# Performance work log

Hardware: AMD Instinct MI355X
Metric: run time of the kernel (lower is better)

The kernel has to match this reference:

```python
import jax, jax.numpy as jnp
import numpy as np

B, S, D, H = 8, 128, 256, 8
T = S + 1
HD = D // H  # head_dim = 32
GAMMA = 1.0
NEG_INF = -1e9
LN_EPS = 1e-5


def setup_inputs() -> dict:
    key = jax.random.key(0)
    ks = jax.random.split(key, 16)
    sc = 0.05
    return {
        "desc_embeddings": jax.random.normal(ks[0], (B, S, D), jnp.float32),
        "name_value_embeddings": jax.random.normal(ks[1], (B, T, D), jnp.float32),
        "prior_Q": jax.random.uniform(ks[2], (B, H, S, S), jnp.float32),
        "Wq": jax.random.normal(ks[3], (D, D), jnp.float32) * sc,
        "bq": jnp.zeros((D,), jnp.float32),
        "Wk": jax.random.normal(ks[4], (D, D), jnp.float32) * sc,
        "bk": jnp.zeros((D,), jnp.float32),
        "Wv": jax.random.normal(ks[5], (D, D), jnp.float32) * sc,
        "bv": jnp.zeros((D,), jnp.float32),
        "wa": jax.random.normal(ks[6], (3 * HD,), jnp.float32) * sc,  # attn_proj weight (out=1)
        "ba": jnp.zeros((), jnp.float32),
        "We1": jax.random.normal(ks[7], (2 * D, D), jnp.float32) * sc,
        "be1": jnp.zeros((D,), jnp.float32),
        "ln_g": jnp.ones((D,), jnp.float32),
        "ln_b": jnp.zeros((D,), jnp.float32),
        "We2": jax.random.normal(ks[8], (D, D), jnp.float32) * sc,
        "be2": jnp.zeros((D,), jnp.float32),
    }


def _layer_norm(x, g, b):
    mu = jnp.mean(x, axis=-1, keepdims=True)
    var = jnp.mean(jnp.square(x - mu), axis=-1, keepdims=True)
    return (x - mu) * jax.lax.rsqrt(var + LN_EPS) * g + b


def _heads(x, W, b):  # [B,T,D] -> [B,H,T,HD]
    return (x @ W + b).reshape(B, T, H, HD).transpose(0, 2, 1, 3)


def reference(desc_embeddings, name_value_embeddings, prior_Q,
              Wq, bq, Wk, bk, Wv, bv, wa, ba,
              We1, be1, ln_g, ln_b, We2, be2):
    # structural adjacency (same for every batch element): CLS->Var on, Var->CLS off,
    # Var-Var fully connected without self-loops
    adj = jnp.zeros((T, T), jnp.float32)
    adj = adj.at[1:, 1:].set(1.0 - jnp.eye(S, dtype=jnp.float32))
    adj = adj.at[0, 1:].set(1.0)

    q = _heads(name_value_embeddings, Wq, bq)  # [B,H,T,HD]
    k = _heads(name_value_embeddings, Wk, bk)
    v = _heads(name_value_embeddings, Wv, bv)

    # edge attributes: pairwise concat of desc embeddings, CLS rows/cols use [desc,desc]
    desc = desc_embeddings
    var_edge = jnp.concatenate([
        jnp.broadcast_to(desc[:, :, None, :], (B, S, S, D)),
        jnp.broadcast_to(desc[:, None, :, :], (B, S, S, D)),
    ], axis=-1)  # [B,S,S,2D]
    cls_edge = jnp.concatenate([desc, desc], axis=-1)  # [B,S,2D]
    edge = jnp.zeros((B, T, T, 2 * D), jnp.float32)
    edge = edge.at[:, 1:, 1:].set(var_edge)
    edge = edge.at[:, 0, 1:].set(cls_edge)
    edge = edge.at[:, 1:, 0].set(cls_edge)

    # edge_update MLP: Linear(2D->D) -> LayerNorm -> ReLU -> Linear(D->D)
    h = jax.nn.relu(_layer_norm(edge @ We1 + be1, ln_g, ln_b)) @ We2 + be2  # [B,T,T,D]
    # split into heads, mask by adjacency: [B,H,T,T,HD]
    edge_h = h.reshape(B, T, T, H, HD).transpose(0, 3, 1, 2, 4)
    edge_h = edge_h * adj[None, None, :, :, None]

    # gat_v1 + attn_proj(cat[q_i, k_j, e_ij]) is linear -> decompose to avoid
    # materializing the [B,H,T,T,3*HD] concat
    wa_q, wa_k, wa_e = wa[:HD], wa[HD:2 * HD], wa[2 * HD:]
    logits = (jnp.einsum('bhid,d->bhi', q, wa_q)[:, :, :, None]
              + jnp.einsum('bhjd,d->bhj', k, wa_k)[:, :, None, :]
              + jnp.einsum('bhijd,d->bhij', edge_h, wa_e)
              + ba)  # [B,H,T,T]

    # prior_Q logit-bias injection on Var-Var block
    eps = 1e-6
    p = jnp.clip(prior_Q, eps, 1.0 - eps)
    bias = (jnp.log(p) - jnp.log(1.0 - p)) * GAMMA  # [B,H,S,S]
    logits = logits.at[:, :, 1:, 1:].add(bias)

    # structural mask as pre-softmax -inf
    logits = logits + (adj == 0).astype(logits.dtype)[None, None] * NEG_INF

    attn = jax.nn.softmax(logits, axis=-1)  # [B,H,T,T]
    ctx = jnp.einsum('bhij,bhjd->bhid', attn, v)  # [B,H,T,HD]
    basis_outputs = ctx.transpose(0, 2, 1, 3)  # [B,T,H,HD]
    return basis_outputs, attn
```

## Files before the change

### kernel.cpp

```cpp
#include <hip/hip_runtime.h>
#include <math.h>

#define B 8
#define S 128
#define D 256
#define H 8
#define T 129
#define HD 32
#define NEG_INF -1000000000.0f
#define LN_EPS 1e-5f

__global__ __launch_bounds__(256) void gemm_all(
    const float* __restrict__ nv, const float* __restrict__ desc,
    const float* __restrict__ Wq, const float* __restrict__ bq,
    const float* __restrict__ Wk, const float* __restrict__ bk,
    const float* __restrict__ Wv, const float* __restrict__ bv,
    const float* __restrict__ We1, const float* __restrict__ be1,
    const float* __restrict__ We2, const float* __restrict__ be2,
    const float* __restrict__ wa,
    float* __restrict__ v, float* __restrict__ U, float* __restrict__ V,
    float* __restrict__ Vt, float* __restrict__ qdkd,
    float* __restrict__ W2aT, float* __restrict__ econst,
    float* __restrict__ sU, float* __restrict__ sU2,
    float* __restrict__ sV, float* __restrict__ sV2)
{
    const int blk = blockIdx.x;
    const int tid = threadIdx.x;

    __shared__ float xs16[16 * 260];
    __shared__ float wq_s[4096];
    __shared__ float bq_s[16];
    __shared__ float red[4][8];

    if (blk < 770) {
        const float* X; const float* W; const float* bias; int r0; int mode;
        if (blk < 258)      { X = nv;   W = Wv;        bias = bv;      r0 = blk * 4;         mode = 0; }
        else if (blk < 514) { X = desc; W = We1;       bias = be1;     r0 = (blk - 258) * 4; mode = 1; }
        else                { X = desc; W = We1 + D*D; bias = nullptr; r0 = (blk - 514) * 4; mode = 2; }
        const int c = tid;

        const float* x0 = X + (r0 + 0) * D;
        const float* x1 = X + (r0 + 1) * D;
        const float* x2 = X + (r0 + 2) * D;
        const float* x3 = X + (r0 + 3) * D;

        float acc0 = 0.f, acc1 = 0.f, acc2 = 0.f, acc3 = 0.f;
        float w[8], nw[8];
        #pragma unroll
        for (int q = 0; q < 8; ++q) w[q] = W[q * D + c];

        for (int kk = 0; kk < 256; kk += 8) {
            const int kn = kk + 8;
            if (kn < 256) {
                #pragma unroll
                for (int q = 0; q < 8; ++q) nw[q] = W[(kn + q) * D + c];
            }
            float xv0[8], xv1[8], xv2[8], xv3[8];
            *(float4*)&xv0[0] = *(const float4*)(x0 + kk);
            *(float4*)&xv0[4] = *(const float4*)(x0 + kk + 4);
            *(float4*)&xv1[0] = *(const float4*)(x1 + kk);
            *(float4*)&xv1[4] = *(const float4*)(x1 + kk + 4);
            *(float4*)&xv2[0] = *(const float4*)(x2 + kk);
            *(float4*)&xv2[4] = *(const float4*)(x2 + kk + 4);
            *(float4*)&xv3[0] = *(const float4*)(x3 + kk);
            *(float4*)&xv3[4] = *(const float4*)(x3 + kk + 4);
            #pragma unroll
            for (int q = 0; q < 8; ++q) {
                acc0 = fmaf(xv0[q], w[q], acc0);
                acc1 = fmaf(xv1[q], w[q], acc1);
                acc2 = fmaf(xv2[q], w[q], acc2);
                acc3 = fmaf(xv3[q], w[q], acc3);
            }
            if (kn < 256) {
                #pragma unroll
                for (int q = 0; q < 8; ++q) w[q] = nw[q];
            }
        }

        const float bb = bias ? bias[c] : 0.f;
        const float o0 = acc0 + bb, o1 = acc1 + bb, o2 = acc2 + bb, o3 = acc3 + bb;

        if (mode == 0) {
            if (r0 + 0 < B*T) v[(r0 + 0) * D + c] = o0;
            if (r0 + 1 < B*T) v[(r0 + 1) * D + c] = o1;
            if (r0 + 2 < B*T) v[(r0 + 2) * D + c] = o2;
            if (r0 + 3 < B*T) v[(r0 + 3) * D + c] = o3;
        } else {
            if (mode == 1) {
                U[(r0 + 0) * D + c] = o0;
                U[(r0 + 1) * D + c] = o1;
                U[(r0 + 2) * D + c] = o2;
                U[(r0 + 3) * D + c] = o3;
            } else {
                V[(r0 + 0) * D + c] = o0;
                V[(r0 + 1) * D + c] = o1;
                V[(r0 + 2) * D + c] = o2;
                V[(r0 + 3) * D + c] = o3;
                const int b_ = r0 >> 7, rl = r0 & 127;
                float4 tv; tv.x = o0; tv.y = o1; tv.z = o2; tv.w = o3;
                *(float4*)&Vt[((size_t)b_ * D + c) * S + rl] = tv;
            }
            float s0 = o0, s1 = o1, s2 = o2, s3 = o3;
            float q0 = o0*o0, q1 = o1*o1, q2 = o2*o2, q3 = o3*o3;
            #pragma unroll
            for (int m = 32; m >= 1; m >>= 1) {
                s0 += __shfl_xor(s0, m); q0 += __shfl_xor(q0, m);
                s1 += __shfl_xor(s1, m); q1 += __shfl_xor(q1, m);
                s2 += __shfl_xor(s2, m); q2 += __shfl_xor(q2, m);
                s3 += __shfl_xor(s3, m); q3 += __shfl_xor(q3, m);
            }
            const int wv = tid >> 6;
            if ((tid & 63) == 0) {
                red[wv][0] = s0; red[wv][1] = s1; red[wv][2] = s2; red[wv][3] = s3;
                red[wv][4] = q0; red[wv][5] = q1; red[wv][6] = q2; red[wv][7] = q3;
            }
            __syncthreads();
            if (tid < 4) {
                const float ss = red[0][tid] + red[1][tid] + red[2][tid] + red[3][tid];
                const float qq = red[0][4+tid] + red[1][4+tid] + red[2][4+tid] + red[3][4+tid];
                const int row = r0 + tid;
                if (mode == 1) { sU[row] = ss; sU2[row] = qq; }
                else           { sV[row] = ss; sV2[row] = qq; }
            }
        }
    } else if (blk < 835) {
        const int r0 = (blk - 770) * 16;
        for (int t = tid; t < 4096; t += 256) {
            const int k = t >> 4, cc = t & 15;
            const float* Wsrc = (cc < 8) ? Wq : Wk;
            const float* wap  = (cc < 8) ? wa : wa + HD;
            const int h = cc & 7;
            float s = 0.f;
            #pragma unroll
            for (int d = 0; d < HD; ++d) s = fmaf(Wsrc[k*D + h*HD + d], wap[d], s);
            wq_s[t] = s;
        }
        if (tid < 16) {
            const float* bsrc = (tid < 8) ? bq : bk;
            const float* wap  = (tid < 8) ? wa : wa + HD;
            const int h = tid & 7;
            float s = 0.f;
            #pragma unroll
            for (int d = 0; d < HD; ++d) s = fmaf(bsrc[h*HD + d], wap[d], s);
            bq_s[tid] = s;
        }
        for (int t = tid; t < 16 * 256; t += 256) {
            const int r = t >> 8, cch = t & 255, rr = r0 + r;
            xs16[r * 260 + cch] = (rr < B*T) ? nv[rr * D + cch] : 0.f;
        }
        __syncthreads();

        const int r = tid >> 4, cc = tid & 15;
        float acc = 0.f;
        for (int kk = 0; kk < 256; kk += 4) {
            const float4 x = *(const float4*)&xs16[r * 260 + kk];
            acc = fmaf(x.x, wq_s[(kk+0)*16 + cc], acc);
            acc = fmaf(x.y, wq_s[(kk+1)*16 + cc], acc);
            acc = fmaf(x.z, wq_s[(kk+2)*16 + cc], acc);
            acc = fmaf(x.w, wq_s[(kk+3)*16 + cc], acc);
        }
        const int rr = r0 + r;
        if (rr < B*T) qdkd[rr * 16 + cc] = acc + bq_s[cc];
    } else {
        for (int t = tid; t < 2048; t += 256) {
            const int h = t >> 8, cch = t & 255;
            float s = 0.f;
            #pragma unroll
            for (int d = 0; d < HD; ++d) s = fmaf(We2[cch*D + h*HD + d], wa[2*HD + d], s);
            W2aT[h*D + cch] = s;
        }
        if (tid < 8) {
            float s = 0.f;
            #pragma unroll
            for (int d = 0; d < HD; ++d) s = fmaf(be2[tid*HD + d], wa[2*HD + d], s);
            econst[tid] = s;
        }
    }
}

__global__ __launch_bounds__(256) void uv_gemm(
    const float* __restrict__ U, const float* __restrict__ Vt,
    float* __restrict__ UV)
{
    const int br = blockIdx.x;
    const int b  = br >> 7;
    const int j  = threadIdx.x & 127, kh = threadIdx.x >> 7;
    const float* urow = U + (size_t)br * D + kh * 128;
    const float* vt   = Vt + (size_t)b * D * S + (size_t)kh * 128 * S;

    float acc = 0.f;
    #pragma unroll 8
    for (int c = 0; c < 128; c += 4) {
        const float4 u4 = *(const float4*)(urow + c);
        acc = fmaf(u4.x, vt[(c+0)*S + j], acc);
        acc = fmaf(u4.y, vt[(c+1)*S + j], acc);
        acc = fmaf(u4.z, vt[(c+2)*S + j], acc);
        acc = fmaf(u4.w, vt[(c+3)*S + j], acc);
    }
    __shared__ float part[2][128];
    part[kh][j] = acc;
    __syncthreads();
    if (kh == 0) UV[(size_t)br * S + j] = part[0][j] + part[1][j];
}

__global__ __launch_bounds__(512) void edge_attn(
    const float* __restrict__ U, const float* __restrict__ V,
    const float* __restrict__ W2aT, const float* __restrict__ econst,
    const float* __restrict__ ln_g, const float* __restrict__ ln_b,
    const float* __restrict__ qdkd, const float* __restrict__ prior,
    const float* __restrict__ v, const float* __restrict__ ba,
    const float* __restrict__ sU, const float* __restrict__ sU2,
    const float* __restrict__ sV, const float* __restrict__ sV2,
    const float* __restrict__ UV,
    float* __restrict__ out_basis, float* __restrict__ out_attn)
{
    const int bid = blockIdx.x;
    const int b = bid / T, i = bid % T;
    const int tid = threadIdx.x, lane = tid & 63, wid = tid >> 6;
    const int c0 = lane * 4;

    __shared__ float escl[H][132];
    __shared__ float pat[H][132];

    const float4 g4 = *(const float4*)(ln_g + c0);
    const float4 b4 = *(const float4*)(ln_b + c0);
    float4 w[H];
    #pragma unroll
    for (int h = 0; h < H; ++h) w[h] = *(const float4*)(W2aT + h*D + c0);
    float4 u4i = make_float4(0.f, 0.f, 0.f, 0.f);
    float su_i = 0.f, su2_i = 0.f;
    const float* UVrow = UV;
    if (i >= 1) {
        u4i   = *(const float4*)(U + (size_t)(b*S + (i-1))*D + c0);
        su_i  = sU [b*S + i-1];
        su2_i = sU2[b*S + i-1];
        UVrow = UV + (size_t)(b*S + (i-1))*S;
    }

    const int hmap = 4*(lane&1) + 2*((lane>>1)&1) + ((lane>>2)&1);
    const float ecl = (lane < 8) ? econst[hmap] : 0.f;

    const int j0 = 1 + wid * 16;
    for (int jj = 0; jj < 16; ++jj) {
        const int j = j0 + jj;
        if (i >= 1 && j == i) continue;

        const float svj  = sV [b*S + j-1];
        const float sv2j = sV2[b*S + j-1];
        float suv, su2v, cross;
        if (i >= 1) {
            suv = su_i; su2v = su2_i;
            cross = UVrow[j-1];
        } else {
            suv   = sU [b*S + j-1];
            su2v  = sU2[b*S + j-1];
            cross = UV[(size_t)(b*S + j-1)*S + (j-1)];
        }
        const float mu  = (suv + svj) * (1.f / D);
        const float ey2 = fmaf(2.f, cross, su2v + sv2j) * (1.f / D);
        const float rs  = rsqrtf(ey2 - mu*mu + LN_EPS);

        const float4 v4 = *(const float4*)(V + (size_t)(b*S + (j-1))*D + c0);
        float4 u4;
        if (i == 0) u4 = *(const float4*)(U + (size_t)(b*S + (j-1))*D + c0);
        else        u4 = u4i;

        const float y0 = u4.x + v4.x, y1 = u4.y + v4.y;
        const float y2 = u4.z + v4.z, y3 = u4.w + v4.w;

        const float t0 = fmaxf((y0 - mu) * rs * g4.x + b4.x, 0.f);
        const float t1 = fmaxf((y1 - mu) * rs * g4.y + b4.y, 0.f);
        const float t2 = fmaxf((y2 - mu) * rs * g4.z + b4.z, 0.f);
        const float t3 = fmaxf((y3 - mu) * rs * g4.w + b4.w, 0.f);

        float ph[H];
        #pragma unroll
        for (int h = 0; h < H; ++h)
            ph[h] = fmaf(t0, w[h].x, fmaf(t1, w[h].y, fmaf(t2, w[h].z, t3 * w[h].w)));

        {
            const bool hi = (lane & 1);
            float k0 = hi ? ph[4] : ph[0], d0 = hi ? ph[0] : ph[4];
            float k1 = hi ? ph[5] : ph[1], d1 = hi ? ph[1] : ph[5];
            float k2 = hi ? ph[6] : ph[2], d2 = hi ? ph[2] : ph[6];
            float k3 = hi ? ph[7] : ph[3], d3 = hi ? ph[3] : ph[7];
            ph[0] = k0 + __shfl_xor(d0, 1);
            ph[1] = k1 + __shfl_xor(d1, 1);
            ph[2] = k2 + __shfl_xor(d2, 1);
            ph[3] = k3 + __shfl_xor(d3, 1);
        }
        {
            const bool hi = (lane & 2);
            float k0 = hi ? ph[2] : ph[0], d0 = hi ? ph[0] : ph[2];
            float k1 = hi ? ph[3] : ph[1], d1 = hi ? ph[1] : ph[3];
            ph[0] = k0 + __shfl_xor(d0, 2);
            ph[1] = k1 + __shfl_xor(d1, 2);
        }
        {
            const bool hi = (lane & 4);
            float k0 = hi ? ph[1] : ph[0], d0 = hi ? ph[0] : ph[1];
            ph[0] = k0 + __shfl_xor(d0, 4);
        }
        ph[0] += __shfl_xor(ph[0], 8);
        ph[0] += __shfl_xor(ph[0], 16);
        ph[0] += __shfl_xor(ph[0], 32);

        if (lane < 8) escl[hmap][j] = ph[0] + ecl;
    }
    __syncthreads();

    const int h = wid;
    const int bh = b*H + h;
    const float qdv = qdkd[(b*T + i)*16 + h];
    const float ba0 = ba[0];
    const int j1 = 1 + lane, j2 = 65 + lane;
    const bool v1 = !(i >= 1 && j1 == i);
    const bool v2 = !(i >= 1 && j2 == i);

    float l1 = NEG_INF, l2 = NEG_INF;
    if (v1) {
        l1 = qdv + qdkd[(b*T + j1)*16 + 8 + h] + escl[h][j1] + ba0;
        if (i >= 1) {
            float pr = prior[((size_t)bh*S + (i-1))*S + (j1-1)];
            pr = fminf(fmaxf(pr, 1e-6f), 1.f - 1e-6f);
            l1 += __logf(pr) - __logf(1.f - pr);
        }
    }
    if (v2) {
        l2 = qdv + qdkd[(b*T + j2)*16 + 8 + h] + escl[h][j2] + ba0;
        if (i >= 1) {
            float pr = prior[((size_t)bh*S + (i-1))*S + (j2-1)];
            pr = fminf(fmaxf(pr, 1e-6f), 1.f - 1e-6f);
            l2 += __logf(pr) - __logf(1.f - pr);
        }
    }

    float m = fmaxf(l1, l2);
    #pragma unroll
    for (int mm = 32; mm >= 1; mm >>= 1) m = fmaxf(m, __shfl_xor(m, mm));
    const float e1 = v1 ? __expf(l1 - m) : 0.f;
    const float e2 = v2 ? __expf(l2 - m) : 0.f;
    float s = e1 + e2;
    #pragma unroll
    for (int mm = 32; mm >= 1; mm >>= 1) s += __shfl_xor(s, mm);
    const float inv = 1.f / s;
    const float at1 = e1 * inv, at2 = e2 * inv;

    float* arow = out_attn + (size_t)(bh*T + i)*T;
    arow[j1] = at1;
    arow[j2] = at2;
    if (lane == 0) arow[0] = 0.f;
    pat[h][j1] = at1;
    pat[h][j2] = at2;
    __syncthreads();

    const int d = lane & 31, half = lane >> 5;
    float acc = 0.f;
    const float* vb = v + (size_t)(b*T)*D + h*HD + d;
    #pragma unroll 8
    for (int jj = 0; jj < 64; ++jj) {
        const int jc = 1 + half*64 + jj;
        acc = fmaf(pat[h][jc], vb[(size_t)jc * D], acc);
    }
    acc += __shfl_xor(acc, 32);
    if (lane < 32)
        out_basis[((size_t)(b*T + i)*H + h)*HD + d] = acc;
}

extern "C" void kernel_launch(void* const* d_in, const int* in_sizes, int n_in,
                              void* d_out, int out_size, void* d_ws, size_t ws_size,
                              hipStream_t stream) {
    const float* desc  = (const float*)d_in[0];
    const float* nv    = (const float*)d_in[1];
    const float* prior = (const float*)d_in[2];
    const float* Wq  = (const float*)d_in[3];
    const float* bq  = (const float*)d_in[4];
    const float* Wk  = (const float*)d_in[5];
    const float* bk  = (const float*)d_in[6];
    const float* Wv  = (const float*)d_in[7];
    const float* bv  = (const float*)d_in[8];
    const float* wa  = (const float*)d_in[9];
    const float* ba  = (const float*)d_in[10];
    const float* We1 = (const float*)d_in[11];
    const float* be1 = (const float*)d_in[12];
    const float* lng = (const float*)d_in[13];
    const float* lnb = (const float*)d_in[14];
    const float* We2 = (const float*)d_in[15];
    const float* be2 = (const float*)d_in[16];

    float* ws = (float*)d_ws;
    float* U    = ws; ws += B*S*D;
    float* V    = ws; ws += B*S*D;
    float* Vt   = ws; ws += B*D*S;
    float* v    = ws; ws += B*T*D;
    float* qdkd = ws; ws += B*T*16;
    float* W2aT = ws; ws += H*D;
    float* ec   = ws; ws += H;
    float* sU   = ws; ws += B*S;
    float* sU2  = ws; ws += B*S;
    float* sV   = ws; ws += B*S;
    float* sV2  = ws; ws += B*S;
    float* UV   = ws; ws += B*S*S;

    float* out_basis = (float*)d_out;
    float* out_attn  = out_basis + B*T*H*HD;

    gemm_all<<<dim3(836), 256, 0, stream>>>(nv, desc, Wq, bq, Wk, bk, Wv, bv,
                                            We1, be1, We2, be2, wa,
                                            v, U, V, Vt, qdkd, W2aT, ec,
                                            sU, sU2, sV, sV2);
    uv_gemm<<<dim3(B*S), 256, 0, stream>>>(U, Vt, UV);
    edge_attn<<<dim3(B*T), 512, 0, stream>>>(U, V, W2aT, ec, lng, lnb,
                                             qdkd, prior, v, ba,
                                             sU, sU2, sV, sV2, UV,
                                             out_basis, out_attn);
}
```

Baseline: 179.8 us.

## Fuse UV cross-term GEMM into edge_attn and process two edges per wavefront

Removes the separate uv_gemm launch and its UV workspace. Each edge_attn block now computes its own row of U·V cross terms (or the diagonal for the CLS row) into shared memory. The edge loop is restructured so each half-wavefront handles a different j with 8 channels per lane, and W2 is stored channel-major so lanes load contiguous weights. This saves one launch and a global round trip for UV. In exchange each block redoes a 256x128 dot-product row from Vt, and register pressure rises under the launch bound of 4 blocks.

Measured after the change: 183.7 us. 1.02x slower.

```diff
diff --git a/kernel.cpp b/kernel.cpp
--- a/kernel.cpp
+++ b/kernel.cpp
@@ -20,7 +20,7 @@
     const float* __restrict__ wa,
     float* __restrict__ v, float* __restrict__ U, float* __restrict__ V,
     float* __restrict__ Vt, float* __restrict__ qdkd,
-    float* __restrict__ W2aT, float* __restrict__ econst,
+    float* __restrict__ W2ca, float* __restrict__ econst,
     float* __restrict__ sU, float* __restrict__ sU2,
     float* __restrict__ sV, float* __restrict__ sV2)
 {
@@ -163,11 +163,11 @@
         if (rr < B*T) qdkd[rr * 16 + cc] = acc + bq_s[cc];
     } else {
         for (int t = tid; t < 2048; t += 256) {
-            const int h = t >> 8, cch = t & 255;
+            const int cch = t >> 3, h = t & 7;
             float s = 0.f;
             #pragma unroll
             for (int d = 0; d < HD; ++d) s = fmaf(We2[cch*D + h*HD + d], wa[2*HD + d], s);
-            W2aT[h*D + cch] = s;
+            W2ca[t] = s;
         }
         if (tid < 8) {
             float s = 0.f;
@@ -178,135 +178,205 @@
     }
 }
 
-__global__ __launch_bounds__(256) void uv_gemm(
-    const float* __restrict__ U, const float* __restrict__ Vt,
-    float* __restrict__ UV)
-{
-    const int br = blockIdx.x;
-    const int b  = br >> 7;
-    const int j  = threadIdx.x & 127, kh = threadIdx.x >> 7;
-    const float* urow = U + (size_t)br * D + kh * 128;
-    const float* vt   = Vt + (size_t)b * D * S + (size_t)kh * 128 * S;
-
-    float acc = 0.f;
-    #pragma unroll 8
-    for (int c = 0; c < 128; c += 4) {
-        const float4 u4 = *(const float4*)(urow + c);
-        acc = fmaf(u4.x, vt[(c+0)*S + j], acc);
-        acc = fmaf(u4.y, vt[(c+1)*S + j], acc);
-        acc = fmaf(u4.z, vt[(c+2)*S + j], acc);
-        acc = fmaf(u4.w, vt[(c+3)*S + j], acc);
-    }
-    __shared__ float part[2][128];
-    part[kh][j] = acc;
-    __syncthreads();
-    if (kh == 0) UV[(size_t)br * S + j] = part[0][j] + part[1][j];
-}
-
-__global__ __launch_bounds__(512) void edge_attn(
+__global__ __launch_bounds__(512, 4) void edge_attn(
     const float* __restrict__ U, const float* __restrict__ V,
-    const float* __restrict__ W2aT, const float* __restrict__ econst,
+    const float* __restrict__ Vt,
+    const float* __restrict__ W2ca, const float* __restrict__ econst,
     const float* __restrict__ ln_g, const float* __restrict__ ln_b,
     const float* __restrict__ qdkd, const float* __restrict__ prior,
     const float* __restrict__ v, const float* __restrict__ ba,
     const float* __restrict__ sU, const float* __restrict__ sU2,
     const float* __restrict__ sV, const float* __restrict__ sV2,
-    const float* __restrict__ UV,
     float* __restrict__ out_basis, float* __restrict__ out_attn)
 {
     const int bid = blockIdx.x;
     const int b = bid / T, i = bid % T;
     const int tid = threadIdx.x, lane = tid & 63, wid = tid >> 6;
-    const int c0 = lane * 4;
+    const int lane32 = lane & 31, half = lane >> 5;
+    const int c0 = lane32 * 8;
 
     __shared__ float escl[H][132];
     __shared__ float pat[H][132];
-
-    const float4 g4 = *(const float4*)(ln_g + c0);
-    const float4 b4 = *(const float4*)(ln_b + c0);
-    float4 w[H];
+    __shared__ float uvp[4][128];
+    __shared__ float uvrow[128];
+
+    {
+        const int j = tid & 127, kc = tid >> 7;
+        float a = 0.f;
+        if (i >= 1) {
+            const float* ur = U + (size_t)(b*S + (i-1))*D + kc*64;
+            const float* vt = Vt + ((size_t)b*D + kc*64)*S + j;
+            #pragma unroll 4
+            for (int c = 0; c < 64; c += 4) {
+                const float4 u4 = *(const float4*)(ur + c);
+                a = fmaf(u4.x, vt[(c+0)*S], a);
+                a = fmaf(u4.y, vt[(c+1)*S], a);
+                a = fmaf(u4.z, vt[(c+2)*S], a);
+                a = fmaf(u4.w, vt[(c+3)*S], a);
+            }
+        } else {
+            const float* ur = U + (size_t)(b*S + j)*D + kc*64;
+            const float* vr = V + (size_t)(b*S + j)*D + kc*64;
+            #pragma unroll 4
+            for (int c = 0; c < 64; c += 4) {
+                const float4 u4 = *(const float4*)(ur + c);
+                const float4 v4 = *(const float4*)(vr + c);
+                a = fmaf(u4.x, v4.x, fmaf(u4.y, v4.y, fmaf(u4.z, v4.z, fmaf(u4.w, v4.w, a))));
+            }
+        }
+        uvp[kc][j] = a;
+    }
+    __syncthreads();
+    if (tid < 128) uvrow[tid] = uvp[0][tid] + uvp[1][tid] + uvp[2][tid] + uvp[3][tid];
+    __syncthreads();
+
+    float g_[8], b_[8];
+    *(float4*)&g_[0] = *(const float4*)(ln_g + c0);
+    *(float4*)&g_[4] = *(const float4*)(ln_g + c0 + 4);
+    *(float4*)&b_[0] = *(const float4*)(ln_b + c0);
+    *(float4*)&b_[4] = *(const float4*)(ln_b + c0 + 4);
+    float4 w2a[8], w2b[8];
     #pragma unroll
-    for (int h = 0; h < H; ++h) w[h] = *(const float4*)(W2aT + h*D + c0);
-    float4 u4i = make_float4(0.f, 0.f, 0.f, 0.f);
+    for (int cc = 0; cc < 8; ++cc) {
+        w2a[cc] = *(const float4*)(W2ca + (c0 + cc)*8);
+        w2b[cc] = *(const float4*)(W2ca + (c0 + cc)*8 + 4);
+    }
+    float ua[8];
     float su_i = 0.f, su2_i = 0.f;
-    const float* UVrow = UV;
     if (i >= 1) {
-        u4i   = *(const float4*)(U + (size_t)(b*S + (i-1))*D + c0);
+        const float* urow = U + (size_t)(b*S + (i-1))*D + c0;
+        *(float4*)&ua[0] = *(const float4*)(urow);
+        *(float4*)&ua[4] = *(const float4*)(urow + 4);
         su_i  = sU [b*S + i-1];
         su2_i = sU2[b*S + i-1];
-        UVrow = UV + (size_t)(b*S + (i-1))*S;
-    }
-
-    const int hmap = 4*(lane&1) + 2*((lane>>1)&1) + ((lane>>2)&1);
-    const float ecl = (lane < 8) ? econst[hmap] : 0.f;
-
-    const int j0 = 1 + wid * 16;
-    for (int jj = 0; jj < 16; ++jj) {
-        const int j = j0 + jj;
-        if (i >= 1 && j == i) continue;
-
-        const float svj  = sV [b*S + j-1];
-        const float sv2j = sV2[b*S + j-1];
-        float suv, su2v, cross;
-        if (i >= 1) {
-            suv = su_i; su2v = su2_i;
-            cross = UVrow[j-1];
-        } else {
-            suv   = sU [b*S + j-1];
-            su2v  = sU2[b*S + j-1];
-            cross = UV[(size_t)(b*S + j-1)*S + (j-1)];
-        }
-        const float mu  = (suv + svj) * (1.f / D);
-        const float ey2 = fmaf(2.f, cross, su2v + sv2j) * (1.f / D);
-        const float rs  = rsqrtf(ey2 - mu*mu + LN_EPS);
-
-        const float4 v4 = *(const float4*)(V + (size_t)(b*S + (j-1))*D + c0);
-        float4 u4;
-        if (i == 0) u4 = *(const float4*)(U + (size_t)(b*S + (j-1))*D + c0);
-        else        u4 = u4i;
-
-        const float y0 = u4.x + v4.x, y1 = u4.y + v4.y;
-        const float y2 = u4.z + v4.z, y3 = u4.w + v4.w;
-
-        const float t0 = fmaxf((y0 - mu) * rs * g4.x + b4.x, 0.f);
-        const float t1 = fmaxf((y1 - mu) * rs * g4.y + b4.y, 0.f);
-        const float t2 = fmaxf((y2 - mu) * rs * g4.z + b4.z, 0.f);
-        const float t3 = fmaxf((y3 - mu) * rs * g4.w + b4.w, 0.f);
-
-        float ph[H];
+    }
+
+    const int hmap = 4*(lane32&1) + 2*((lane32>>1)&1) + ((lane32>>2)&1);
+    const float ecl = (lane32 < 8) ? econst[hmap] : 0.f;
+
+    const int j0 = 1 + wid * 16 + half;
+#define PHASE_A(UEXPR, SU, SU2)                                               \
+    _Pragma("unroll")                                                         \
+    for (int step = 0; step < 8; ++step) {                                    \
+        const int j = j0 + step * 2;                                          \
+        const float svj  = sV [b*S + j-1];                                    \
+        const float sv2j = sV2[b*S + j-1];                                    \
+        const float cross = uvrow[j-1];                                       \
+        const float mu  = ((SU) + svj) * (1.f / D);                           \
+        const float ey2 = fmaf(2.f, cross, (SU2) + sv2j) * (1.f / D);         \
+        const float rs  = rsqrtf(ey2 - mu*mu + LN_EPS);                       \
+        float vv[8];                                                          \
+        const float* vrow = V + (size_t)(b*S + (j-1))*D + c0;                 \
+        *(float4*)&vv[0] = *(const float4*)(vrow);                            \
+        *(float4*)&vv[4] = *(const float4*)(vrow + 4);                       \
+        float ph[8] = {0.f,0.f,0.f,0.f,0.f,0.f,0.f,0.f};                      \
+        _Pragma("unroll")                                                     \
+        for (int cc = 0; cc < 8; ++cc) {                                      \
+            const float y = (UEXPR) + vv[cc];                                 \
+            float t = fmaf((y - mu) * rs, g_[cc], b_[cc]);                    \
+            t = fmaxf(t, 0.f);                                                \
+            ph[0] = fmaf(t, w2a[cc].x, ph[0]);                                \
+            ph[1] = fmaf(t, w2a[cc].y, ph[1]);                                \
+            ph[2] = fmaf(t, w2a[cc].z, ph[2]);                                \
+            ph[3] = fmaf(t, w2a[cc].w, ph[3]);                                \
+            ph[4] = fmaf(t, w2b[cc].x, ph[4]);                                \
+            ph[5] = fmaf(t, w2b[cc].y, ph[5]);                                \
+            ph[6] = fmaf(t, w2b[cc].z, ph[6]);                                \
+            ph[7] = fmaf(t, w2b[cc].w, ph[7]);                                \
+        }                                                                     \
+        {                                                                     \
+            const bool hi = (lane32 & 1);                                     \
+            float k0 = hi ? ph[4] : ph[0], d0 = hi ? ph[0] : ph[4];           \
+            float k1 = hi ? ph[5] : ph[1], d1 = hi ? ph[1] : ph[5];           \
+            float k2 = hi ? ph[6] : ph[2], d2 = hi ? ph[2] : ph[6];           \
+            float k3 = hi ? ph[7] : ph[3], d3 = hi ? ph[3] : ph[7];           \
+            ph[0] = k0 + __shfl_xor(d0, 1);                                   \
+            ph[1] = k1 + __shfl_xor(d1, 1);                                   \
+            ph[2] = k2 + __shfl_xor(d2, 1);                                   \
+            ph[3] = k3 + __shfl_xor(d3, 1);                                   \
+        }                                                                     \
+        {                                                                     \
+            const bool hi = (lane32 & 2);                                     \
+            float k0 = hi ? ph[2] : ph[0], d0 = hi ? ph[0] : ph[2];           \
+            float k1 = hi ? ph[3] : ph[1], d1 = hi ? ph[1] : ph[3];           \
+            ph[0] = k0 + __shfl_xor(d0, 2);                                   \
+            ph[1] = k1 + __shfl_xor(d1, 2);                                   \
+        }                                                                     \
+        {                                                                     \
+            const bool hi = (lane32 & 4);                                     \
+            float k0 = hi ? ph[1] : ph[0], d0 = hi ? ph[0] : ph[1];           \
+            ph[0] = k0 + __shfl_xor(d0, 4);                                   \
+        }                                                                     \
+        ph[0] += __shfl_xor(ph[0], 8);                                        \
+        ph[0] += __shfl_xor(ph[0], 16);                                       \
+        if (lane32 < 8) escl[hmap][j] = ph[0] + ecl;                          \
+    }
+
+    if (i >= 1) {
+        PHASE_A(ua[cc], su_i, su2_i)
+    } else {
         #pragma unroll
-        for (int h = 0; h < H; ++h)
-            ph[h] = fmaf(t0, w[h].x, fmaf(t1, w[h].y, fmaf(t2, w[h].z, t3 * w[h].w)));
-
-        {
-            const bool hi = (lane & 1);
-            float k0 = hi ? ph[4] : ph[0], d0 = hi ? ph[0] : ph[4];
-            float k1 = hi ? ph[5] : ph[1], d1 = hi ? ph[1] : ph[5];
-            float k2 = hi ? ph[6] : ph[2], d2 = hi ? ph[2] : ph[6];
-            float k3 = hi ? ph[7] : ph[3], d3 = hi ? ph[3] : ph[7];
-            ph[0] = k0 + __shfl_xor(d0, 1);
-            ph[1] = k1 + __shfl_xor(d1, 1);
-            ph[2] = k2 + __shfl_xor(d2, 1);
-            ph[3] = k3 + __shfl_xor(d3, 1);
-        }
-        {
-            const bool hi = (lane & 2);
-            float k0 = hi ? ph[2] : ph[0], d0 = hi ? ph[0] : ph[2];
-            float k1 = hi ? ph[3] : ph[1], d1 = hi ? ph[1] : ph[3];
-            ph[0] = k0 + __shfl_xor(d0, 2);
-            ph[1] = k1 + __shfl_xor(d1, 2);
-        }
-        {
-            const bool hi = (lane & 4);
-            float k0 = hi ? ph[1] : ph[0], d0 = hi ? ph[0] : ph[1];
-            ph[0] = k0 + __shfl_xor(d0, 4);
-        }
-        ph[0] += __shfl_xor(ph[0], 8);
-        ph[0] += __shfl_xor(ph[0], 16);
-        ph[0] += __shfl_xor(ph[0], 32);
-
-        if (lane < 8) escl[hmap][j] = ph[0] + ecl;
-    }
+        for (int step = 0; step < 8; ++step) {
+            const int j = j0 + step * 2;
+            const float svj  = sV [b*S + j-1];
+            const float sv2j = sV2[b*S + j-1];
+            const float suj  = sU [b*S + j-1];
+            const float su2j = sU2[b*S + j-1];
+            const float cross = uvrow[j-1];
+            const float mu  = (suj + svj) * (1.f / D);
+            const float ey2 = fmaf(2.f, cross, su2j + sv2j) * (1.f / D);
+            const float rs  = rsqrtf(ey2 - mu*mu + LN_EPS);
+            float vv[8], uu[8];
+            const float* vrow = V + (size_t)(b*S + (j-1))*D + c0;
+            const float* urow = U + (size_t)(b*S + (j-1))*D + c0;
+            *(float4*)&vv[0] = *(const float4*)(vrow);
+            *(float4*)&vv[4] = *(const float4*)(vrow + 4);
+            *(float4*)&uu[0] = *(const float4*)(urow);
+            *(float4*)&uu[4] = *(const float4*)(urow + 4);
+            float ph[8] = {0.f,0.f,0.f,0.f,0.f,0.f,0.f,0.f};
+            #pragma unroll
+            for (int cc = 0; cc < 8; ++cc) {
+                const float y = uu[cc] + vv[cc];
+                float t = fmaf((y - mu) * rs, g_[cc], b_[cc]);
+                t = fmaxf(t, 0.f);
+                ph[0] = fmaf(t, w2a[cc].x, ph[0]);
+                ph[1] = fmaf(t, w2a[cc].y, ph[1]);
+                ph[2] = fmaf(t, w2a[cc].z, ph[2]);
+                ph[3] = fmaf(t, w2a[cc].w, ph[3]);
+                ph[4] = fmaf(t, w2b[cc].x, ph[4]);
+                ph[5] = fmaf(t, w2b[cc].y, ph[5]);
+                ph[6] = fmaf(t, w2b[cc].z, ph[6]);
+                ph[7] = fmaf(t, w2b[cc].w, ph[7]);
+            }
+            {
+                const bool hi = (lane32 & 1);
+                float k0 = hi ? ph[4] : ph[0], d0 = hi ? ph[0] : ph[4];
+                float k1 = hi ? ph[5] : ph[1], d1 = hi ? ph[1] : ph[5];
+                float k2 = hi ? ph[6] : ph[2], d2 = hi ? ph[2] : ph[6];
+                float k3 = hi ? ph[7] : ph[3], d3 = hi ? ph[3] : ph[7];
+                ph[0] = k0 + __shfl_xor(d0, 1);
+                ph[1] = k1 + __shfl_xor(d1, 1);
+                ph[2] = k2 + __shfl_xor(d2, 1);
+                ph[3] = k3 + __shfl_xor(d3, 1);
+            }
+            {
+                const bool hi = (lane32 & 2);
+                float k0 = hi ? ph[2] : ph[0], d0 = hi ? ph[0] : ph[2];
+                float k1 = hi ? ph[3] : ph[1], d1 = hi ? ph[1] : ph[3];
+                ph[0] = k0 + __shfl_xor(d0, 2);
+                ph[1] = k1 + __shfl_xor(d1, 2);
+            }
+            {
+                const bool hi = (lane32 & 4);
+                float k0 = hi ? ph[1] : ph[0], d0 = hi ? ph[0] : ph[1];
+                ph[0] = k0 + __shfl_xor(d0, 4);
+            }
+            ph[0] += __shfl_xor(ph[0], 8);
+            ph[0] += __shfl_xor(ph[0], 16);
+            if (lane32 < 8) escl[hmap][j] = ph[0] + ecl;
+        }
+    }
+#undef PHASE_A
     __syncthreads();
 
     const int h = wid;
@@ -354,12 +424,12 @@
     pat[h][j2] = at2;
     __syncthreads();
 
-    const int d = lane & 31, half = lane >> 5;
+    const int d = lane & 31, halfc = lane >> 5;
     float acc = 0.f;
     const float* vb = v + (size_t)(b*T)*D + h*HD + d;
     #pragma unroll 8
     for (int jj = 0; jj < 64; ++jj) {
-        const int jc = 1 + half*64 + jj;
+        const int jc = 1 + halfc*64 + jj;
         acc = fmaf(pat[h][jc], vb[(size_t)jc * D], acc);
     }
     acc += __shfl_xor(acc, 32);
@@ -394,24 +464,22 @@
     float* Vt   = ws; ws += B*D*S;
     float* v    = ws; ws += B*T*D;
     float* qdkd = ws; ws += B*T*16;
-    float* W2aT = ws; ws += H*D;
+    float* W2ca = ws; ws += D*H;
     float* ec   = ws; ws += H;
     float* sU   = ws; ws += B*S;
     float* sU2  = ws; ws += B*S;
     float* sV   = ws; ws += B*S;
     float* sV2  = ws; ws += B*S;
-    float* UV   = ws; ws += B*S*S;
 
     float* out_basis = (float*)d_out;
     float* out_attn  = out_basis + B*T*H*HD;
 
     gemm_all<<<dim3(836), 256, 0, stream>>>(nv, desc, Wq, bq, Wk, bk, Wv, bv,
                                             We1, be1, We2, be2, wa,
-                                            v, U, V, Vt, qdkd, W2aT, ec,
+                                            v, U, V, Vt, qdkd, W2ca, ec,
                                             sU, sU2, sV, sV2);
-    uv_gemm<<<dim3(B*S), 256, 0, stream>>>(U, Vt, UV);
-    edge_attn<<<dim3(B*T), 512, 0, stream>>>(U, V, W2aT, ec, lng, lnb,
+    edge_attn<<<dim3(B*T), 512, 0, stream>>>(U, V, Vt, W2ca, ec, lng, lnb,
                                              qdkd, prior, v, ba,
-                                             sU, sU2, sV, sV2, UV,
+                                             sU, sU2, sV, sV2,
                                              out_basis, out_attn);
 }
```
